# Performance work log

Measured on AMD Instinct MI355X. Metric: run time of the kernel, lower is better.

The kernel has to match this reference:

```python
import jax, jax.numpy as jnp
import numpy as np

S, B, E, H = 2048, 4, 1024, 16
D = E // H  # head_dim = 64


def setup_inputs() -> dict:
    key = jax.random.key(0)
    k1, k2, k3 = jax.random.split(key, 3)
    # xavier-uniform-ish init scales
    query = jax.random.normal(k1, (S, B, E), dtype=jnp.float32)
    in_proj_weight = jax.random.normal(k2, (3 * E, E), dtype=jnp.float32) * (2.0 / (4 * E)) ** 0.5
    in_proj_bias = jnp.zeros((3 * E,), dtype=jnp.float32)
    out_proj_weight = jax.random.normal(k3, (E, E), dtype=jnp.float32) * (1.0 / E) ** 0.5
    out_proj_bias = jnp.zeros((E,), dtype=jnp.float32)
    return {
        "query": query,
        "in_proj_weight": in_proj_weight,
        "in_proj_bias": in_proj_bias,
        "out_proj_weight": out_proj_weight,
        "out_proj_bias": out_proj_bias,
    }


def reference(query, in_proj_weight, in_proj_bias, out_proj_weight, out_proj_bias):
    # Self-attention path (qkv_same): fused in_proj then chunk into q,k,v.
    # query: (S, B, E); F.linear(x, W, b) = x @ W.T + b
    qkv = jnp.einsum('sbe,fe->sbf', query, in_proj_weight) + in_proj_bias  # (S, B, 3E)
    q, k, v = jnp.split(qkv, 3, axis=-1)  # each (S, B, E)
    scaling = D ** (-0.5)
    q = q * scaling
    # reshape to (B*H, S, D): view(S, B*H, D).transpose(0,1)
    def to_bh(x):
        return x.reshape(S, B * H, D).transpose(1, 0, 2)
    q, k, v = to_bh(q), to_bh(k), to_bh(v)
    # scores: (B*H, S, S)
    scores = jnp.einsum('nqd,nkd->nqk', q, k)
    attn = jax.nn.softmax(scores, axis=-1)  # dropout p=0 (inference)
    out = jnp.einsum('nqk,nkd->nqd', attn, v)  # (B*H, S, D)
    out = out.transpose(1, 0, 2).reshape(S, B, E)
    out = jnp.einsum('sbe,fe->sbf', out, out_proj_weight) + out_proj_bias
    return out
```

## Files before the change

### kernel.cpp

```cpp
#include <hip/hip_runtime.h>
#include <hip/hip_bf16.h>


typedef __attribute__((ext_vector_type(8))) short bf16x8;
typedef __attribute__((ext_vector_type(4))) float floatx4;

#define S_LEN 2048
#define EMB   1024
#define DHEAD 64

static __device__ __forceinline__ unsigned short f2bf(float x) {
    return __builtin_bit_cast(unsigned short, __float2bfloat16(x));
}

static __device__ __forceinline__ void dma16(const void* g, void* l) {
    __builtin_amdgcn_global_load_lds(
        (const __attribute__((address_space(1))) unsigned int*)(unsigned long long)g,
        (__attribute__((address_space(3))) unsigned int*)(unsigned int)(unsigned long long)l,
        16, 0, 0);
}

static __device__ __forceinline__ float red_sum16(float x) {
    x += __int_as_float(__builtin_amdgcn_mov_dpp(__float_as_int(x), 0xB1, 0xF, 0xF, false));
    x += __int_as_float(__builtin_amdgcn_mov_dpp(__float_as_int(x), 0x4E, 0xF, 0xF, false));
    x += __int_as_float(__builtin_amdgcn_mov_dpp(__float_as_int(x), 0x124, 0xF, 0xF, false));
    x += __int_as_float(__builtin_amdgcn_mov_dpp(__float_as_int(x), 0x128, 0xF, 0xF, false));
    return x;
}

__global__ void detect_kernel(const unsigned short* __restrict__ q, int* __restrict__ flag) {
    __shared__ int cnt;
    if (threadIdx.x == 0) cnt = 0;
    __syncthreads();
    int local = 0;
    for (int i = threadIdx.x; i < 4096; i += 256) {
        unsigned short u = q[i];
        int e = (u >> 7) & 0xFF;
        if (e >= 132) local++;
    }
    atomicAdd(&cnt, local);
    __syncthreads();
    if (threadIdx.x == 0) *flag = (cnt > 100) ? 1 : 0;
}

__global__ void convert_all_kernel(
    const void* __restrict__ s0, const void* __restrict__ s1, const void* __restrict__ s2,
    const void* __restrict__ s3, const void* __restrict__ s4,
    __hip_bfloat16* __restrict__ d0, __hip_bfloat16* __restrict__ d1, __hip_bfloat16* __restrict__ d2,
    __hip_bfloat16* __restrict__ d3, __hip_bfloat16* __restrict__ d4,
    const int* __restrict__ flag)
{
    const int mode = *flag;
    const int c0 = 2097152, c1 = c0 + 786432, c2 = c1 + 768, c3 = c2 + 262144, c4 = c3 + 256;
    int i = blockIdx.x * blockDim.x + threadIdx.x;
    const int stride = gridDim.x * blockDim.x;
    for (; i < c4; i += stride) {
        const void* s; __hip_bfloat16* d; int off;
        if (i < c0)      { s = s0; d = d0; off = i; }
        else if (i < c1) { s = s1; d = d1; off = i - c0; }
        else if (i < c2) { s = s2; d = d2; off = i - c1; }
        else if (i < c3) { s = s3; d = d3; off = i - c2; }
        else             { s = s4; d = d4; off = i - c3; }
        if (mode) {
            float4 v = ((const float4*)s)[off];
            ushort4 o;
            o.x = f2bf(v.x); o.y = f2bf(v.y); o.z = f2bf(v.z); o.w = f2bf(v.w);
            ((ushort4*)d)[off] = o;
        } else {
            ((ushort4*)d)[off] = ((const ushort4*)s)[off];
        }
    }
}

#define GEMM_STAGE(As, Bs, Aptr, Bptr, ldA, ldB)                                       \
    {                                                                                  \
        const int srow = (l >> 3);                                                     \
        const int cG   = ((l & 7) ^ srow) * 8;                                         \
        _Pragma("unroll")                                                              \
        for (int j = 0; j < 4; j++) {                                                  \
            const int r0 = wave * 32 + j * 8;                                          \
            dma16(Aptr + (size_t)(r0 + srow) * ldA + cG, &As[r0][0]);                  \
            dma16(Bptr + (size_t)(r0 + srow) * ldB + cG, &Bs[r0][0]);                  \
        }                                                                              \
    }

__global__ __launch_bounds__(256) void qkv_gemm_kernel(
    const __hip_bfloat16* __restrict__ X,
    const __hip_bfloat16* __restrict__ W,
    const __hip_bfloat16* __restrict__ bias,
    __hip_bfloat16* __restrict__ Qws,
    __hip_bfloat16* __restrict__ Kws,
    __hip_bfloat16* __restrict__ Vws)
{
    __shared__ alignas(16) __hip_bfloat16 As[128][64];
    __shared__ alignas(16) __hip_bfloat16 Bs[128][64];

    const int t    = threadIdx.x;
    const int l    = t & 63;
    const int wave = t >> 6;
    const int l15  = l & 15;
    const int quad = l >> 4;
    const int wr   = (wave >> 1) * 64;
    const int wc   = (wave & 1) * 64;
    const int rowBase = blockIdx.x * 128;
    const int colBase = blockIdx.y * 128;

    floatx4 acc[4][4] = {};

    for (int k0 = 0; k0 < EMB; k0 += 64) {
        __syncthreads();
        const __hip_bfloat16* Ap = X + (size_t)rowBase * EMB + k0;
        const __hip_bfloat16* Bp = W + (size_t)colBase * EMB + k0;
        GEMM_STAGE(As, Bs, Ap, Bp, EMB, EMB)
        __syncthreads();
#pragma unroll
        for (int ks = 0; ks < 2; ks++) {
            bf16x8 af[4], bfr[4];
#pragma unroll
            for (int ti = 0; ti < 4; ti++) {
                const int rA = wr + ti * 16 + l15;
                af[ti] = *(const bf16x8*)(&As[rA][(((ks * 4 + quad) ^ (rA & 7)) * 8)]);
            }
#pragma unroll
            for (int tj = 0; tj < 4; tj++) {
                const int rB = wc + tj * 16 + l15;
                bfr[tj] = *(const bf16x8*)(&Bs[rB][(((ks * 4 + quad) ^ (rB & 7)) * 8)]);
            }
#pragma unroll
            for (int ti = 0; ti < 4; ti++)
#pragma unroll
                for (int tj = 0; tj < 4; tj++)
                    acc[ti][tj] = __builtin_amdgcn_mfma_f32_16x16x32_bf16(
                        af[ti], bfr[tj], acc[ti][tj], 0, 0, 0);
        }
    }

    const float QSCALE = 0.125f * 1.44269504088896f;
#pragma unroll
    for (int tj = 0; tj < 4; tj++) {
        const int col = colBase + wc + tj * 16 + l15;
        const int sec = col >> 10;
        const int e   = col & 1023;
        const int h   = e >> 6;
        const int d   = e & 63;
        const float bv = __bfloat162float(bias[col]);
#pragma unroll
        for (int ti = 0; ti < 4; ti++) {
#pragma unroll
            for (int r = 0; r < 4; r++) {
                const int row = rowBase + wr + ti * 16 + quad * 4 + r;
                const int s  = row >> 2;
                const int b  = row & 3;
                const int nh = b * 16 + h;
                const float val = acc[ti][tj][r] + bv;
                if (sec == 0) {
                    Qws[((size_t)nh * S_LEN + s) * DHEAD + d] = __float2bfloat16(val * QSCALE);
                } else if (sec == 1) {
                    Kws[((size_t)nh * S_LEN + s) * DHEAD + d] = __float2bfloat16(val);
                } else {
                    Vws[((size_t)nh * DHEAD + d) * S_LEN + s] = __float2bfloat16(val);
                }
            }
        }
    }
}

__global__ __launch_bounds__(256, 4) void attn_kernel(
    const __hip_bfloat16* __restrict__ Qws,
    const __hip_bfloat16* __restrict__ Kws,
    const __hip_bfloat16* __restrict__ Vws,
    __hip_bfloat16* __restrict__ AOut)
{
    __shared__ alignas(16) __hip_bfloat16 Ks[64][64];
    __shared__ alignas(16) __hip_bfloat16 Vts[64][64];
    __shared__ alignas(16) __hip_bfloat16 Ps[4][32][72];

    const int n  = blockIdx.x;
    const int q0 = blockIdx.y * 128;
    const int t    = threadIdx.x;
    const int l    = t & 63;
    const int wave = t >> 6;
    const int l15  = l & 15;
    const int quad = l >> 4;

    bf16x8 qa[2][2];
#pragma unroll
    for (int qs = 0; qs < 2; qs++)
#pragma unroll
        for (int ks = 0; ks < 2; ks++)
            qa[qs][ks] = *(const bf16x8*)(Qws +
                ((size_t)n * S_LEN + q0 + wave * 32 + qs * 16 + l15) * DHEAD + ks * 32 + quad * 8);

    floatx4 o[2][4] = {};
    float lsum[2][4] = {};

    const int srow = (l >> 3);
    const int cG   = ((l & 7) ^ srow) * 8;

    for (int kt = 0; kt < 32; kt++) {
        __syncthreads();
        const int key0 = kt * 64;
#pragma unroll
        for (int j = 0; j < 2; j++) {
            const int r0 = wave * 16 + j * 8;
            dma16(Kws + ((size_t)n * S_LEN + key0 + r0 + srow) * DHEAD + cG, &Ks[r0][0]);
            dma16(Vws + ((size_t)n * DHEAD + r0 + srow) * S_LEN + key0 + cG, &Vts[r0][0]);
        }
        __syncthreads();

        floatx4 sacc[2][4] = {};
#pragma unroll
        for (int ks = 0; ks < 2; ks++) {
#pragma unroll
            for (int nt = 0; nt < 4; nt++) {
                const int rK = nt * 16 + l15;
                bf16x8 kb = *(const bf16x8*)(&Ks[rK][(((ks * 4 + quad) ^ (rK & 7)) * 8)]);
#pragma unroll
                for (int qs = 0; qs < 2; qs++)
                    sacc[qs][nt] = __builtin_amdgcn_mfma_f32_16x16x32_bf16(
                        qa[qs][ks], kb, sacc[qs][nt], 0, 0, 0);
            }
        }

#pragma unroll
        for (int qs = 0; qs < 2; qs++) {
#pragma unroll
            for (int r = 0; r < 4; r++) {
                float pv[4];
#pragma unroll
                for (int nt = 0; nt < 4; nt++)
                    pv[nt] = __builtin_amdgcn_exp2f(sacc[qs][nt][r]);
                lsum[qs][r] += (pv[0] + pv[1]) + (pv[2] + pv[3]);
#pragma unroll
                for (int nt = 0; nt < 4; nt++)
                    Ps[wave][qs * 16 + quad * 4 + r][nt * 16 + l15] = __float2bfloat16(pv[nt]);
            }
        }

        bf16x8 pa[2][2];
#pragma unroll
        for (int qs = 0; qs < 2; qs++)
#pragma unroll
            for (int ks = 0; ks < 2; ks++)
                pa[qs][ks] = *(const bf16x8*)(&Ps[wave][qs * 16 + l15][ks * 32 + quad * 8]);
#pragma unroll
        for (int ks = 0; ks < 2; ks++) {
#pragma unroll
            for (int nt = 0; nt < 4; nt++) {
                const int rV = nt * 16 + l15;
                bf16x8 vb = *(const bf16x8*)(&Vts[rV][(((ks * 4 + quad) ^ (rV & 7)) * 8)]);
#pragma unroll
                for (int qs = 0; qs < 2; qs++)
                    o[qs][nt] = __builtin_amdgcn_mfma_f32_16x16x32_bf16(
                        pa[qs][ks], vb, o[qs][nt], 0, 0, 0);
            }
        }
    }

    const int bb  = n >> 4;
    const int h64 = (n & 15) * 64;
#pragma unroll
    for (int qs = 0; qs < 2; qs++) {
#pragma unroll
        for (int r = 0; r < 4; r++) {
            const float linv = 1.0f / red_sum16(lsum[qs][r]);
#pragma unroll
            for (int nt = 0; nt < 4; nt++) {
                const int q = q0 + wave * 32 + qs * 16 + quad * 4 + r;
                const int d = nt * 16 + l15;
                AOut[((size_t)q * 4 + bb) * EMB + h64 + d] = __float2bfloat16(o[qs][nt][r] * linv);
            }
        }
    }
}

__global__ __launch_bounds__(256) void out_gemm_kernel(
    const __hip_bfloat16* __restrict__ A,
    const __hip_bfloat16* __restrict__ W,
    const __hip_bfloat16* __restrict__ bias,
    void* __restrict__ out,
    const int* __restrict__ flag)
{
    __shared__ alignas(16) __hip_bfloat16 As[128][64];
    __shared__ alignas(16) __hip_bfloat16 Bs[128][64];

    const int t    = threadIdx.x;
    const int l    = t & 63;
    const int wave = t >> 6;
    const int l15  = l & 15;
    const int quad = l >> 4;
    const int wr   = (wave >> 1) * 64;
    const int wc   = (wave & 1) * 64;
    const int rowBase = blockIdx.x * 128;
    const int colBase = blockIdx.y * 128;
    const int mode = *flag;

    floatx4 acc[4][4] = {};

    for (int k0 = 0; k0 < EMB; k0 += 64) {
        __syncthreads();
        const __hip_bfloat16* Ap = A + (size_t)rowBase * EMB + k0;
        const __hip_bfloat16* Bp = W + (size_t)colBase * EMB + k0;
        GEMM_STAGE(As, Bs, Ap, Bp, EMB, EMB)
        __syncthreads();
#pragma unroll
        for (int ks = 0; ks < 2; ks++) {
            bf16x8 af[4], bfr[4];
#pragma unroll
            for (int ti = 0; ti < 4; ti++) {
                const int rA = wr + ti * 16 + l15;
                af[ti] = *(const bf16x8*)(&As[rA][(((ks * 4 + quad) ^ (rA & 7)) * 8)]);
            }
#pragma unroll
            for (int tj = 0; tj < 4; tj++) {
                const int rB = wc + tj * 16 + l15;
                bfr[tj] = *(const bf16x8*)(&Bs[rB][(((ks * 4 + quad) ^ (rB & 7)) * 8)]);
            }
#pragma unroll
            for (int ti = 0; ti < 4; ti++)
#pragma unroll
                for (int tj = 0; tj < 4; tj++)
                    acc[ti][tj] = __builtin_amdgcn_mfma_f32_16x16x32_bf16(
                        af[ti], bfr[tj], acc[ti][tj], 0, 0, 0);
        }
    }

#pragma unroll
    for (int tj = 0; tj < 4; tj++) {
        const int col = colBase + wc + tj * 16 + l15;
        const float bv = __bfloat162float(bias[col]);
#pragma unroll
        for (int ti = 0; ti < 4; ti++) {
#pragma unroll
            for (int r = 0; r < 4; r++) {
                const int row = rowBase + wr + ti * 16 + quad * 4 + r;
                const float val = acc[ti][tj][r] + bv;
                if (mode) {
                    ((float*)out)[(size_t)row * EMB + col] = val;
                } else {
                    ((__hip_bfloat16*)out)[(size_t)row * EMB + col] = __float2bfloat16(val);
                }
            }
        }
    }
}

extern "C" void kernel_launch(void* const* d_in, const int* in_sizes, int n_in,
                              void* d_out, int out_size, void* d_ws, size_t ws_size,
                              hipStream_t stream) {
    const void* query = d_in[0];
    const void* w_in  = d_in[1];
    const void* b_in  = d_in[2];
    const void* w_out = d_in[3];
    const void* b_out = d_in[4];

    char* ws = (char*)d_ws;
    int*            flag   = (int*)ws;
    __hip_bfloat16* Xc     = (__hip_bfloat16*)(ws + 256);
    __hip_bfloat16* Winc   = Xc   + (size_t)8192 * 1024;
    __hip_bfloat16* binc   = Winc + (size_t)3072 * 1024;
    __hip_bfloat16* Woutc  = binc + 3072;
    __hip_bfloat16* boutc  = Woutc + (size_t)1024 * 1024;
    __hip_bfloat16* Qws    = boutc + 1024;
    __hip_bfloat16* Kws    = Qws + (size_t)8388608;
    __hip_bfloat16* Vws    = Kws + (size_t)8388608;
    __hip_bfloat16* AOut   = Vws + (size_t)8388608;

    detect_kernel<<<1, 256, 0, stream>>>((const unsigned short*)query, flag);

    convert_all_kernel<<<2048, 256, 0, stream>>>(query, w_in, b_in, w_out, b_out,
                                                 Xc, Winc, binc, Woutc, boutc, flag);

    qkv_gemm_kernel<<<dim3(64, 24), 256, 0, stream>>>(Xc, Winc, binc, Qws, Kws, Vws);
    attn_kernel<<<dim3(64, 16), 256, 0, stream>>>(Qws, Kws, Vws, AOut);
    out_gemm_kernel<<<dim3(64, 8), 256, 0, stream>>>(AOut, Woutc, boutc, d_out, flag);
}
```

Measured before the change: 294.2 us.

## Split QKV GEMM into per-section launches and double key tile in attention

The single QKV projection kernel becomes a template over the section (Q, K or V), launched three times, so the per-element output branch is resolved at compile time. The attention kernel now loads 128 keys per iteration into two 64-key LDS buffers, which halves the number of barrier pairs. Its occupancy hint drops from 4 to 3 blocks per CU. The trade-off is two extra kernel launches, more LDS per block, and lower occupancy in attention.

```diff
diff --git a/kernel.cpp b/kernel.cpp
--- a/kernel.cpp
+++ b/kernel.cpp
@@ -84,13 +84,12 @@
         }                                                                              \
     }
 
+template <int SEC>
 __global__ __launch_bounds__(256) void qkv_gemm_kernel(
     const __hip_bfloat16* __restrict__ X,
     const __hip_bfloat16* __restrict__ W,
     const __hip_bfloat16* __restrict__ bias,
-    __hip_bfloat16* __restrict__ Qws,
-    __hip_bfloat16* __restrict__ Kws,
-    __hip_bfloat16* __restrict__ Vws)
+    __hip_bfloat16* __restrict__ Dst)
 {
     __shared__ alignas(16) __hip_bfloat16 As[128][64];
     __shared__ alignas(16) __hip_bfloat16 Bs[128][64];
@@ -103,7 +102,8 @@
     const int wr   = (wave >> 1) * 64;
     const int wc   = (wave & 1) * 64;
     const int rowBase = blockIdx.x * 128;
-    const int colBase = blockIdx.y * 128;
+    const int colSec  = blockIdx.y * 128;
+    const int colBase = SEC * 1024 + colSec;
 
     floatx4 acc[4][4] = {};
 
@@ -138,12 +138,10 @@
     const float QSCALE = 0.125f * 1.44269504088896f;
 #pragma unroll
     for (int tj = 0; tj < 4; tj++) {
-        const int col = colBase + wc + tj * 16 + l15;
-        const int sec = col >> 10;
-        const int e   = col & 1023;
-        const int h   = e >> 6;
-        const int d   = e & 63;
-        const float bv = __bfloat162float(bias[col]);
+        const int e = colSec + wc + tj * 16 + l15;
+        const int h = e >> 6;
+        const int d = e & 63;
+        const float bv = __bfloat162float(bias[SEC * 1024 + e]);
 #pragma unroll
         for (int ti = 0; ti < 4; ti++) {
 #pragma unroll
@@ -153,26 +151,26 @@
                 const int b  = row & 3;
                 const int nh = b * 16 + h;
                 const float val = acc[ti][tj][r] + bv;
-                if (sec == 0) {
-                    Qws[((size_t)nh * S_LEN + s) * DHEAD + d] = __float2bfloat16(val * QSCALE);
-                } else if (sec == 1) {
-                    Kws[((size_t)nh * S_LEN + s) * DHEAD + d] = __float2bfloat16(val);
+                if constexpr (SEC == 0) {
+                    Dst[((size_t)nh * S_LEN + s) * DHEAD + d] = __float2bfloat16(val * QSCALE);
+                } else if constexpr (SEC == 1) {
+                    Dst[((size_t)nh * S_LEN + s) * DHEAD + d] = __float2bfloat16(val);
                 } else {
-                    Vws[((size_t)nh * DHEAD + d) * S_LEN + s] = __float2bfloat16(val);
-                }
-            }
-        }
-    }
-}
-
-__global__ __launch_bounds__(256, 4) void attn_kernel(
+                    Dst[((size_t)nh * DHEAD + d) * S_LEN + s] = __float2bfloat16(val);
+                }
+            }
+        }
+    }
+}
+
+__global__ __launch_bounds__(256, 3) void attn_kernel(
     const __hip_bfloat16* __restrict__ Qws,
     const __hip_bfloat16* __restrict__ Kws,
     const __hip_bfloat16* __restrict__ Vws,
     __hip_bfloat16* __restrict__ AOut)
 {
-    __shared__ alignas(16) __hip_bfloat16 Ks[64][64];
-    __shared__ alignas(16) __hip_bfloat16 Vts[64][64];
+    __shared__ alignas(16) __hip_bfloat16 Ks[2][64][64];
+    __shared__ alignas(16) __hip_bfloat16 Vts[2][64][64];
     __shared__ alignas(16) __hip_bfloat16 Ps[4][32][72];
 
     const int n  = blockIdx.x;
@@ -197,62 +195,70 @@
     const int srow = (l >> 3);
     const int cG   = ((l & 7) ^ srow) * 8;
 
-    for (int kt = 0; kt < 32; kt++) {
-        __syncthreads();
-        const int key0 = kt * 64;
-#pragma unroll
-        for (int j = 0; j < 2; j++) {
-            const int r0 = wave * 16 + j * 8;
-            dma16(Kws + ((size_t)n * S_LEN + key0 + r0 + srow) * DHEAD + cG, &Ks[r0][0]);
-            dma16(Vws + ((size_t)n * DHEAD + r0 + srow) * S_LEN + key0 + cG, &Vts[r0][0]);
-        }
-        __syncthreads();
-
-        floatx4 sacc[2][4] = {};
-#pragma unroll
-        for (int ks = 0; ks < 2; ks++) {
-#pragma unroll
-            for (int nt = 0; nt < 4; nt++) {
-                const int rK = nt * 16 + l15;
-                bf16x8 kb = *(const bf16x8*)(&Ks[rK][(((ks * 4 + quad) ^ (rK & 7)) * 8)]);
-#pragma unroll
-                for (int qs = 0; qs < 2; qs++)
-                    sacc[qs][nt] = __builtin_amdgcn_mfma_f32_16x16x32_bf16(
-                        qa[qs][ks], kb, sacc[qs][nt], 0, 0, 0);
-            }
-        }
-
-#pragma unroll
-        for (int qs = 0; qs < 2; qs++) {
-#pragma unroll
-            for (int r = 0; r < 4; r++) {
-                float pv[4];
-#pragma unroll
-                for (int nt = 0; nt < 4; nt++)
-                    pv[nt] = __builtin_amdgcn_exp2f(sacc[qs][nt][r]);
-                lsum[qs][r] += (pv[0] + pv[1]) + (pv[2] + pv[3]);
-#pragma unroll
-                for (int nt = 0; nt < 4; nt++)
-                    Ps[wave][qs * 16 + quad * 4 + r][nt * 16 + l15] = __float2bfloat16(pv[nt]);
-            }
-        }
-
-        bf16x8 pa[2][2];
-#pragma unroll
-        for (int qs = 0; qs < 2; qs++)
-#pragma unroll
-            for (int ks = 0; ks < 2; ks++)
-                pa[qs][ks] = *(const bf16x8*)(&Ps[wave][qs * 16 + l15][ks * 32 + quad * 8]);
-#pragma unroll
-        for (int ks = 0; ks < 2; ks++) {
-#pragma unroll
-            for (int nt = 0; nt < 4; nt++) {
-                const int rV = nt * 16 + l15;
-                bf16x8 vb = *(const bf16x8*)(&Vts[rV][(((ks * 4 + quad) ^ (rV & 7)) * 8)]);
-#pragma unroll
-                for (int qs = 0; qs < 2; qs++)
-                    o[qs][nt] = __builtin_amdgcn_mfma_f32_16x16x32_bf16(
-                        pa[qs][ks], vb, o[qs][nt], 0, 0, 0);
+    for (int kt = 0; kt < 16; kt++) {
+        __syncthreads();
+        const int key0 = kt * 128;
+#pragma unroll
+        for (int hf = 0; hf < 2; hf++) {
+#pragma unroll
+            for (int j = 0; j < 2; j++) {
+                const int r0 = wave * 16 + j * 8;
+                dma16(Kws + ((size_t)n * S_LEN + key0 + hf * 64 + r0 + srow) * DHEAD + cG,
+                      &Ks[hf][r0][0]);
+                dma16(Vws + ((size_t)n * DHEAD + r0 + srow) * S_LEN + key0 + hf * 64 + cG,
+                      &Vts[hf][r0][0]);
+            }
+        }
+        __syncthreads();
+
+#pragma unroll
+        for (int hf = 0; hf < 2; hf++) {
+            floatx4 sacc[2][4] = {};
+#pragma unroll
+            for (int ks = 0; ks < 2; ks++) {
+#pragma unroll
+                for (int nt = 0; nt < 4; nt++) {
+                    const int rK = nt * 16 + l15;
+                    bf16x8 kb = *(const bf16x8*)(&Ks[hf][rK][(((ks * 4 + quad) ^ (rK & 7)) * 8)]);
+#pragma unroll
+                    for (int qs = 0; qs < 2; qs++)
+                        sacc[qs][nt] = __builtin_amdgcn_mfma_f32_16x16x32_bf16(
+                            qa[qs][ks], kb, sacc[qs][nt], 0, 0, 0);
+                }
+            }
+
+#pragma unroll
+            for (int qs = 0; qs < 2; qs++) {
+#pragma unroll
+                for (int r = 0; r < 4; r++) {
+                    float pv[4];
+#pragma unroll
+                    for (int nt = 0; nt < 4; nt++)
+                        pv[nt] = __builtin_amdgcn_exp2f(sacc[qs][nt][r]);
+                    lsum[qs][r] += (pv[0] + pv[1]) + (pv[2] + pv[3]);
+#pragma unroll
+                    for (int nt = 0; nt < 4; nt++)
+                        Ps[wave][qs * 16 + quad * 4 + r][nt * 16 + l15] = __float2bfloat16(pv[nt]);
+                }
+            }
+
+            bf16x8 pa[2][2];
+#pragma unroll
+            for (int qs = 0; qs < 2; qs++)
+#pragma unroll
+                for (int ks = 0; ks < 2; ks++)
+                    pa[qs][ks] = *(const bf16x8*)(&Ps[wave][qs * 16 + l15][ks * 32 + quad * 8]);
+#pragma unroll
+            for (int ks = 0; ks < 2; ks++) {
+#pragma unroll
+                for (int nt = 0; nt < 4; nt++) {
+                    const int rV = nt * 16 + l15;
+                    bf16x8 vb = *(const bf16x8*)(&Vts[hf][rV][(((ks * 4 + quad) ^ (rV & 7)) * 8)]);
+#pragma unroll
+                    for (int qs = 0; qs < 2; qs++)
+                        o[qs][nt] = __builtin_amdgcn_mfma_f32_16x16x32_bf16(
+                            pa[qs][ks], vb, o[qs][nt], 0, 0, 0);
+                }
             }
         }
     }
@@ -371,7 +377,9 @@
     convert_all_kernel<<<2048, 256, 0, stream>>>(query, w_in, b_in, w_out, b_out,
                                                  Xc, Winc, binc, Woutc, boutc, flag);
 
-    qkv_gemm_kernel<<<dim3(64, 24), 256, 0, stream>>>(Xc, Winc, binc, Qws, Kws, Vws);
+    qkv_gemm_kernel<0><<<dim3(64, 8), 256, 0, stream>>>(Xc, Winc, binc, Qws);
+    qkv_gemm_kernel<1><<<dim3(64, 8), 256, 0, stream>>>(Xc, Winc, binc, Kws);
+    qkv_gemm_kernel<2><<<dim3(64, 8), 256, 0, stream>>>(Xc, Winc, binc, Vws);
     attn_kernel<<<dim3(64, 16), 256, 0, stream>>>(Qws, Kws, Vws, AOut);
     out_gemm_kernel<<<dim3(64, 8), 256, 0, stream>>>(AOut, Woutc, boutc, d_out, flag);
 }
```

Result: slower. 307.7 us (+4.6%).
